# Optimization experiments

Hardware: AMD Instinct MI355X
Metric: run time of the kernel (lower is better)

Reference implementation:

```python
import jax, jax.numpy as jnp
import numpy as np

N, E, D_IN, D_OUT, MAX_DEG = 50000, 800000, 128, 128, 64
ALPHA = 0.5


def _linear_params(key, fan_in, fan_out):
    s = 1.0 / np.sqrt(fan_in)
    kw, kb = jax.random.split(key)
    W = jax.random.uniform(kw, (fan_out, fan_in), jnp.float32, -s, s)
    b = jax.random.uniform(kb, (fan_out,), jnp.float32, -s, s)
    return W, b


def setup_inputs() -> dict:
    key = jax.random.key(0)
    ks = jax.random.split(key, 16)
    x = jax.random.normal(ks[0], (N, D_IN), jnp.float32)
    edge_index = jax.random.randint(ks[1], (2, E), 0, N, dtype=jnp.int64)
    in_degree = jax.random.randint(ks[2], (N,), 0, MAX_DEG, dtype=jnp.int64)
    out_degree = jax.random.randint(ks[3], (N,), 0, MAX_DEG, dtype=jnp.int64)
    out_deg_mask = jax.random.uniform(ks[4], (N,), jnp.float32)
    out_deg_mask_bias = jax.random.uniform(ks[5], (N,), jnp.float32)
    in_deg_mask = jax.random.uniform(ks[6], (N,), jnp.float32)
    in_deg_mask_bias = jax.random.uniform(ks[7], (N,), jnp.float32)
    W_src, b_src = _linear_params(ks[8], D_IN, D_OUT)
    W_dst, b_dst = _linear_params(ks[9], D_IN, D_OUT)
    W_out_f, b_out_f = _linear_params(ks[10], D_IN, 1)
    W_in_f, b_in_f = _linear_params(ks[11], D_IN, 1)
    W_fc, b_fc = _linear_params(ks[12], D_IN, D_OUT)
    # degree embedding tables, padding_idx=0 -> row 0 zeroed
    in_deg_table = (jax.random.normal(ks[13], (MAX_DEG, D_IN), jnp.float32)).at[0].set(0.0)
    out_deg_table = (jax.random.normal(ks[14], (MAX_DEG, D_IN), jnp.float32)).at[0].set(0.0)
    return {
        "x": x, "edge_index": edge_index,
        "in_degree": in_degree, "out_degree": out_degree,
        "out_deg_mask": out_deg_mask, "out_deg_mask_bias": out_deg_mask_bias,
        "in_deg_mask": in_deg_mask, "in_deg_mask_bias": in_deg_mask_bias,
        "W_src": W_src, "b_src": b_src, "W_dst": W_dst, "b_dst": b_dst,
        "W_out_f": W_out_f, "b_out_f": b_out_f, "W_in_f": W_in_f, "b_in_f": b_in_f,
        "W_fc": W_fc, "b_fc": b_fc,
        "in_deg_table": in_deg_table, "out_deg_table": out_deg_table,
    }


def reference(x, edge_index, in_degree, out_degree,
              out_deg_mask, out_deg_mask_bias, in_deg_mask, in_deg_mask_bias,
              W_src, b_src, W_dst, b_dst,
              W_out_f, b_out_f, W_in_f, b_in_f,
              W_fc, b_fc, in_deg_table, out_deg_table):
    n = x.shape[0]
    row, col = edge_index[0], edge_index[1]
    ones = jnp.ones(row.shape[0], x.dtype)
    # directed norm D_out^{-1/2} A D_in^{-1/2}; transpose reuses the same edge weights
    out_deg = jax.ops.segment_sum(ones, row, num_segments=n)
    in_deg = jax.ops.segment_sum(ones, col, num_segments=n)
    o_inv = jnp.where(out_deg > 0, jax.lax.rsqrt(jnp.maximum(out_deg, 1e-12)), 0.0)
    i_inv = jnp.where(in_deg > 0, jax.lax.rsqrt(jnp.maximum(in_deg, 1e-12)), 0.0)
    w = o_inv[row] * i_inv[col]  # [E]
    # adj_norm @ x and adj_t_norm @ x (SpMM via gather + segment_sum)
    out_nei = jax.ops.segment_sum(w[:, None] * x[col], row, num_segments=n)  # [N,D]
    in_nei = jax.ops.segment_sum(w[:, None] * x[row], col, num_segments=n)   # [N,D]
    # degree-gated filter
    c_out = (out_nei - x + out_deg_table[out_degree]) @ W_out_f.T + b_out_f  # [N,1]
    c_in = (in_nei - x + in_deg_table[in_degree]) @ W_in_f.T + b_in_f        # [N,1]
    C = jax.nn.softmax(jnp.concatenate([c_out, c_in], axis=1), axis=1)        # tau_softmax, tau=1
    C_out = C[:, 0:1] * out_deg_mask[:, None] + out_deg_mask_bias[:, None]
    C_in = C[:, 1:2] * in_deg_mask[:, None] + in_deg_mask_bias[:, None]
    out = (C_out * (out_nei @ W_src.T + b_src)
           + C_in * (in_nei @ W_dst.T + b_dst)
           + ALPHA * (x @ W_fc.T + b_fc))
    return out, C_in, C_out
```

## Files before the change

kernel.cpp:

```cpp
#include <hip/hip_runtime.h>

#define NN 50000
#define EE 800000
#define DD 128
#define CAP 48
#define MT 64
#define XSL 6250
#define PB 128
#define PCB (8 * PB)

typedef short short8_t __attribute__((ext_vector_type(8)));
typedef float f32x4 __attribute__((ext_vector_type(4)));
typedef float f32x2 __attribute__((ext_vector_type(2)));

__device__ __forceinline__ unsigned short f2bf(float f) {
    union { float f; unsigned int i; } v; v.f = f;
    unsigned int x = v.i;
    x += 0x7FFFu + ((x >> 16) & 1u);
    return (unsigned short)(x >> 16);
}
__device__ __forceinline__ unsigned int pack2(float a, float b) {
    return (unsigned int)f2bf(a) | ((unsigned int)f2bf(b) << 16);
}
__device__ __forceinline__ f32x2 bfup(unsigned int u) {
    union { unsigned int i; float f; } lo, hi;
    lo.i = u << 16;
    hi.i = u & 0xFFFF0000u;
    f32x2 r; r.x = lo.f; r.y = hi.f;
    return r;
}
__device__ __forceinline__ void pkfma(f32x2& a, f32x2 b, f32x2 w) {
    asm("v_pk_fma_f32 %0, %1, %2, %0" : "+v"(a) : "v"(b), "v"(w));
}
__device__ __forceinline__ void accw(f32x2* ac, uint4 u, float w) {
    f32x2 wp; wp.x = w; wp.y = w;
    pkfma(ac[0], bfup(u.x), wp); pkfma(ac[1], bfup(u.y), wp);
    pkfma(ac[2], bfup(u.z), wp); pkfma(ac[3], bfup(u.w), wp);
}

__global__ void __launch_bounds__(256) k_pc(
    const int* __restrict__ ei, int* __restrict__ cnt,
    unsigned short* __restrict__ bkt_row, unsigned short* __restrict__ bkt_col,
    const float* __restrict__ x,
    const float* __restrict__ W_src, const float* __restrict__ W_dst,
    const float* __restrict__ W_fc,
    unsigned short* __restrict__ xb, unsigned short* __restrict__ wbf)
{
    if (blockIdx.x < PCB) {
        int xcd = blockIdx.x & 7;
        int b   = blockIdx.x >> 3;
        int lo = xcd * XSL, hi = lo + XSL;
        for (int e = b * 256 + threadIdx.x; e < EE; e += PB * 256) {
            int r = __builtin_nontemporal_load(ei + e);
            int c = __builtin_nontemporal_load(ei + EE + e);
            if (r >= lo && r < hi) {
                int po = atomicAdd(&cnt[r], 1);
                if (po < CAP) bkt_row[(size_t)r * CAP + po] = (unsigned short)c;
            }
            if (c >= lo && c < hi) {
                int pi = atomicAdd(&cnt[NN + c], 1);
                if (pi < CAP) bkt_col[(size_t)c * CAP + pi] = (unsigned short)r;
            }
        }
    } else {
        int t = (blockIdx.x - PCB) * 256 + threadIdx.x;
        int base = t * 4;
        if (base < NN * DD) {
            float4 v = *(const float4*)(x + base);
            uint2 p; p.x = pack2(v.x, v.y); p.y = pack2(v.z, v.w);
            *(uint2*)(xb + base) = p;
        } else {
            int b2 = base - NN * DD;
            if (b2 < 3 * 16384) {
                int src = b2 >> 14;
                int off = b2 & 16383;
                const float* W = (src == 0) ? W_src : (src == 1) ? W_dst : W_fc;
                float sc = (src == 2) ? 0.5f : 1.0f;
                float4 v = *(const float4*)(W + off);
                uint2 p; p.x = pack2(v.x * sc, v.y * sc); p.y = pack2(v.z * sc, v.w * sc);
                *(uint2*)(wbf + b2) = p;
            }
        }
    }
}

__global__ void __launch_bounds__(256) k_gather(
    const uint4* __restrict__ xb4, const float4* __restrict__ x4,
    const unsigned short* __restrict__ bkt_row, const unsigned short* __restrict__ bkt_col,
    const int* __restrict__ cnt,
    const int* __restrict__ in_degree, const int* __restrict__ out_degree,
    const float* __restrict__ odm, const float* __restrict__ odmb,
    const float* __restrict__ idm, const float* __restrict__ idmb,
    const float4* __restrict__ W_out_f4, const float* __restrict__ b_out_f,
    const float4* __restrict__ W_in_f4, const float* __restrict__ b_in_f,
    const float4* __restrict__ in_tab4, const float4* __restrict__ out_tab4,
    uint2* __restrict__ onb2, uint2* __restrict__ inb2,
    float* __restrict__ scbuf,
    float* __restrict__ outCin, float* __restrict__ outCout)
{
    __shared__ float4 sred[2][4][2][16][3];
    __shared__ float sg[2][2];
    __shared__ float sC[2][2];
    int half = threadIdx.x >> 7;
    int n = blockIdx.x * 2 + half;
    int t = threadIdx.x & 127;
    int g = t >> 5;
    int l = t & 31;
    int dir = g >> 1;
    int gd  = g & 1;
    int sub = l >> 4;
    int li  = l & 15;
    int shamt = gd << 4;

    const unsigned short* bp = ((dir == 0) ? bkt_row : bkt_col) + (size_t)n * CAP;
    const int* wcnt = (dir == 0) ? (cnt + NN) : cnt;
    int rawdeg = cnt[dir * NN + n];
    int deg = (rawdeg > CAP) ? CAP : rawdeg;

    unsigned int bw = (l < 24) ? *(const unsigned int*)(bp + 2 * l) : 0u;

    float w_l = 0.0f;
    {
        unsigned int pr = __shfl(bw, l >> 1, 32);
        int il = (pr >> ((l & 1) << 4)) & 0xffff;
        if (l < deg) w_l = 1.0f / sqrtf((float)wcnt[il]);
    }

    f32x2 ac[4];
    ac[0] = (f32x2)0.0f; ac[1] = (f32x2)0.0f; ac[2] = (f32x2)0.0f; ac[3] = (f32x2)0.0f;

    if (deg <= 32) {
        int j = gd;
        for (; j + 14 < deg; j += 16) {
            int s0 = j + 2 * sub, s1 = s0 + 4, s2 = s0 + 8, s3 = s0 + 12;
            int i0 = (__shfl(bw, s0 >> 1, 32) >> shamt) & 0xffff;
            int i1 = (__shfl(bw, s1 >> 1, 32) >> shamt) & 0xffff;
            int i2 = (__shfl(bw, s2 >> 1, 32) >> shamt) & 0xffff;
            int i3 = (__shfl(bw, s3 >> 1, 32) >> shamt) & 0xffff;
            uint4 u0 = xb4[(size_t)i0 * 16 + li];
            uint4 u1 = xb4[(size_t)i1 * 16 + li];
            uint4 u2 = xb4[(size_t)i2 * 16 + li];
            uint4 u3 = xb4[(size_t)i3 * 16 + li];
            float w0 = __shfl(w_l, s0, 32);
            float w1 = __shfl(w_l, s1, 32);
            float w2v = __shfl(w_l, s2, 32);
            float w3 = __shfl(w_l, s3, 32);
            accw(ac, u0, w0); accw(ac, u1, w1); accw(ac, u2, w2v); accw(ac, u3, w3);
        }
        for (; j + 6 < deg; j += 8) {
            int s0 = j + 2 * sub, s1 = s0 + 4;
            int i0 = (__shfl(bw, s0 >> 1, 32) >> shamt) & 0xffff;
            int i1 = (__shfl(bw, s1 >> 1, 32) >> shamt) & 0xffff;
            uint4 u0 = xb4[(size_t)i0 * 16 + li];
            uint4 u1 = xb4[(size_t)i1 * 16 + li];
            float w0 = __shfl(w_l, s0, 32);
            float w1 = __shfl(w_l, s1, 32);
            accw(ac, u0, w0); accw(ac, u1, w1);
        }
        for (; j < deg; j += 4) {
            int s0 = j + 2 * sub;
            int sc = (s0 < deg) ? s0 : gd;
            int i0 = (__shfl(bw, sc >> 1, 32) >> shamt) & 0xffff;
            float w0 = __shfl(w_l, sc, 32);
            if (s0 < deg) {
                uint4 u0 = xb4[(size_t)i0 * 16 + li];
                accw(ac, u0, w0);
            }
        }
    } else {
        for (int j = gd; j < deg; j += 4) {
            int s0 = j + 2 * sub;
            int sc = (s0 < deg) ? s0 : gd;
            int i0 = (__shfl(bw, sc >> 1, 32) >> shamt) & 0xffff;
            if (s0 < deg) {
                float w0 = 1.0f / sqrtf((float)wcnt[i0]);
                uint4 u0 = xb4[(size_t)i0 * 16 + li];
                accw(ac, u0, w0);
            }
        }
    }

    sred[half][g][sub][li][0] = make_float4(ac[0].x, ac[0].y, ac[1].x, ac[1].y);
    sred[half][g][sub][li][1] = make_float4(ac[2].x, ac[2].y, ac[3].x, ac[3].y);
    __syncthreads();

    float4 r = make_float4(0.f, 0.f, 0.f, 0.f);
    if (gd == 0) {
        int src = l >> 1, q = l & 1;
        int g0 = dir * 2;
        float4 b0 = sred[half][g0][0][src][q];
        float4 b1 = sred[half][g0][1][src][q];
        float4 b2 = sred[half][g0 + 1][0][src][q];
        float4 b3 = sred[half][g0 + 1][1][src][q];
        float wn = (rawdeg > 0) ? (1.0f / sqrtf((float)rawdeg)) : 0.0f;
        r.x = wn * (b0.x + b1.x + b2.x + b3.x);
        r.y = wn * (b0.y + b1.y + b2.y + b3.y);
        r.z = wn * (b0.z + b1.z + b2.z + b3.z);
        r.w = wn * (b0.w + b1.w + b2.w + b3.w);
        float4 xv = x4[(size_t)n * 32 + l];
        float4 tb, wf;
        if (dir == 0) {
            int odg = out_degree[n];
            odg = (odg < 0) ? 0 : (odg > 63 ? 63 : odg);
            tb = out_tab4[(size_t)odg * 32 + l];
            wf = W_out_f4[l];
        } else {
            int idg = in_degree[n];
            idg = (idg < 0) ? 0 : (idg > 63 ? 63 : idg);
            tb = in_tab4[(size_t)idg * 32 + l];
            wf = W_in_f4[l];
        }
        float p = (r.x - xv.x + tb.x) * wf.x + (r.y - xv.y + tb.y) * wf.y
                + (r.z - xv.z + tb.z) * wf.z + (r.w - xv.w + tb.w) * wf.w;
        #pragma unroll
        for (int off = 16; off > 0; off >>= 1) p += __shfl_down(p, off);
        if (l == 0) sg[half][dir] = p;
    }
    __syncthreads();
    if (t == 0) {
        float c_out = sg[half][0] + b_out_f[0];
        float c_in  = sg[half][1] + b_in_f[0];
        float m  = fmaxf(c_out, c_in);
        float eo = expf(c_out - m);
        float e2 = expf(c_in  - m);
        float inv = 1.0f / (eo + e2);
        float Cout = (eo * inv) * odm[n] + odmb[n];
        float Cin  = (e2 * inv) * idm[n] + idmb[n];
        sC[half][0] = Cout; sC[half][1] = Cin;
        scbuf[2 * n]     = Cout;
        scbuf[2 * n + 1] = Cin;
        outCout[n] = Cout;
        outCin[n]  = Cin;
    }
    __syncthreads();
    if (gd == 0) {
        float C = sC[half][dir];
        uint2 pw; pw.x = pack2(C * r.x, C * r.y); pw.y = pack2(C * r.z, C * r.w);
        ((dir == 0) ? onb2 : inb2)[(size_t)n * 32 + l] = pw;
    }
}

__global__ void __launch_bounds__(256) k_gemm(
    const unsigned int* __restrict__ xb32,
    const unsigned int* __restrict__ onb32, const unsigned int* __restrict__ inb32,
    const unsigned short* __restrict__ wbf,
    const float* __restrict__ b_src, const float* __restrict__ b_dst,
    const float* __restrict__ b_fc,
    const float* __restrict__ scbuf,
    float* __restrict__ out)
{
    __shared__ unsigned short sA[MT * 72];
    __shared__ unsigned short sBt[DD * 72];

    int tid = threadIdx.x;
    int wid = tid >> 6;
    int lane = tid & 63;
    int ml = lane & 15;
    int kq = lane >> 4;
    int n0 = blockIdx.x * MT;

    f32x4 accv[8];
    #pragma unroll
    for (int i = 0; i < 8; i++) accv[i] = (f32x4)0.0f;

    const unsigned int* srcs[3] = { onb32, inb32, xb32 };

    for (int kt = 0; kt < 6; kt++) {
        int srcsel = kt >> 1;
        int k0 = (kt & 1) * 64;
        const unsigned int* S = srcs[srcsel];

        #pragma unroll
        for (int r = 0; r < 2; r++) {
            int s = tid + 256 * r;
            int row = s >> 3;
            int cg = s & 7;
            int gn = n0 + row;
            uint4 p = make_uint4(0u, 0u, 0u, 0u);
            if (gn < NN) {
                p = *(const uint4*)(S + (size_t)gn * 64 + (k0 >> 1) + cg * 4);
            }
            *(uint4*)(sA + row * 72 + cg * 8) = p;
        }
        #pragma unroll
        for (int r = 0; r < 4; r++) {
            int s = tid + 256 * r;
            int row = s >> 3;
            int cg = s & 7;
            uint4 w = *(const uint4*)(wbf + srcsel * 16384 + row * DD + k0 + cg * 8);
            *(uint4*)(sBt + row * 72 + cg * 8) = w;
        }
        __syncthreads();

        #pragma unroll
        for (int ks = 0; ks < 64; ks += 32) {
            short8_t a = *(const short8_t*)(sA + (16 * wid + ml) * 72 + ks + kq * 8);
            #pragma unroll
            for (int i = 0; i < 8; i++) {
                short8_t b = *(const short8_t*)(sBt + (16 * i + ml) * 72 + ks + kq * 8);
                accv[i] = __builtin_amdgcn_mfma_f32_16x16x32_bf16(a, b, accv[i], 0, 0, 0);
            }
        }
        __syncthreads();
    }

    int row_base = n0 + 16 * wid + 4 * kq;
    #pragma unroll
    for (int r = 0; r < 4; r++) {
        int row = row_base + r;
        if (row >= NN) continue;
        float Cout = scbuf[2 * row];
        float Cin  = scbuf[2 * row + 1];
        #pragma unroll
        for (int i = 0; i < 8; i++) {
            int col = 16 * i + ml;
            out[(size_t)row * DD + col] =
                accv[i][r] + Cout * b_src[col] + Cin * b_dst[col] + 0.5f * b_fc[col];
        }
    }
}

extern "C" void kernel_launch(void* const* d_in, const int* in_sizes, int n_in,
                              void* d_out, int out_size, void* d_ws, size_t ws_size,
                              hipStream_t stream) {
    const float* x    = (const float*)d_in[0];
    const int* ei     = (const int*)d_in[1];
    const int* in_degree  = (const int*)d_in[2];
    const int* out_degree = (const int*)d_in[3];
    const float* odm  = (const float*)d_in[4];
    const float* odmb = (const float*)d_in[5];
    const float* idm  = (const float*)d_in[6];
    const float* idmb = (const float*)d_in[7];
    const float* W_src = (const float*)d_in[8];
    const float* b_src = (const float*)d_in[9];
    const float* W_dst = (const float*)d_in[10];
    const float* b_dst = (const float*)d_in[11];
    const float* W_out_f = (const float*)d_in[12];
    const float* b_out_f = (const float*)d_in[13];
    const float* W_in_f  = (const float*)d_in[14];
    const float* b_in_f  = (const float*)d_in[15];
    const float* W_fc    = (const float*)d_in[16];
    const float* b_fc    = (const float*)d_in[17];
    const float* in_tab  = (const float*)d_in[18];
    const float* out_tab = (const float*)d_in[19];

    unsigned short* xb  = (unsigned short*)d_ws;
    unsigned short* onb = xb + (size_t)NN * DD;
    unsigned short* inb = onb + (size_t)NN * DD;
    float* scbuf = (float*)(inb + (size_t)NN * DD);
    unsigned short* wbf = (unsigned short*)(scbuf + 2 * NN);
    int* cnt     = (int*)(wbf + 3 * 16384);
    unsigned short* bkt_row = (unsigned short*)(cnt + 2 * NN);
    unsigned short* bkt_col = bkt_row + (size_t)NN * CAP;

    hipMemsetAsync(cnt, 0, (size_t)2 * NN * sizeof(int), stream);

    int conv_quads = (NN * DD + 3 * 16384) / 4;
    int conv_blocks = (conv_quads + 255) / 256;
    k_pc<<<PCB + conv_blocks, 256, 0, stream>>>(ei, cnt, bkt_row, bkt_col,
                                                x, W_src, W_dst, W_fc, xb, wbf);

    float* out_p  = (float*)d_out;
    float* cin_p  = out_p + (size_t)NN * DD;
    float* cout_p = cin_p + NN;

    k_gather<<<NN / 2, 256, 0, stream>>>((const uint4*)xb, (const float4*)x,
                                         bkt_row, bkt_col, cnt,
                                         in_degree, out_degree,
                                         odm, odmb, idm, idmb,
                                         (const float4*)W_out_f, b_out_f,
                                         (const float4*)W_in_f, b_in_f,
                                         (const float4*)in_tab, (const float4*)out_tab,
                                         (uint2*)onb, (uint2*)inb,
                                         scbuf, cin_p, cout_p);

    k_gemm<<<(NN + MT - 1) / MT, 256, 0, stream>>>(
        (const unsigned int*)xb, (const unsigned int*)onb, (const unsigned int*)inb,
        wbf, b_src, b_dst, b_fc, scbuf, out_p);
}
```

Before: 282.5 us.

## Merge memset, placement/conversion and gather into one cooperative persistent kernel

Replaces the memset, the edge-bucketing/conversion kernel and the per-node gather kernel with a single cooperative kernel. It zeroes the counters, places edges and converts to bf16, then runs a grid-stride gather loop, with grid.sync between phases. This removes launch gaps and the memset. In exchange the grid is capped at 2048 blocks, fewer than before for the placement and conversion phases, the placement loads lose their nontemporal hints, and grid-wide barriers are added. A fallback to separate kernels is kept in case the cooperative launch fails.

```diff
diff --git a/kernel.cpp b/kernel.cpp
--- a/kernel.cpp
+++ b/kernel.cpp
@@ -1,4 +1,6 @@
 #include <hip/hip_runtime.h>
+#include <hip/hip_cooperative_groups.h>
+namespace cg = cooperative_groups;
 
 #define NN 50000
 #define EE 800000
@@ -6,8 +8,6 @@
 #define CAP 48
 #define MT 64
 #define XSL 6250
-#define PB 128
-#define PCB (8 * PB)
 
 typedef short short8_t __attribute__((ext_vector_type(8)));
 typedef float f32x4 __attribute__((ext_vector_type(4)));
@@ -38,53 +38,62 @@
     pkfma(ac[2], bfup(u.z), wp); pkfma(ac[3], bfup(u.w), wp);
 }
 
-__global__ void __launch_bounds__(256) k_pc(
-    const int* __restrict__ ei, int* __restrict__ cnt,
-    unsigned short* __restrict__ bkt_row, unsigned short* __restrict__ bkt_col,
-    const float* __restrict__ x,
+struct GShared {
+    float4 sred[2][4][2][16][3];
+    float sg[2][2];
+    float sC[2][2];
+};
+
+
+__device__ __forceinline__ void place_phase(
+    int bid, int P, int tid, const int* __restrict__ ei, int* __restrict__ cnt,
+    unsigned short* __restrict__ bkt_row, unsigned short* __restrict__ bkt_col)
+{
+    int xcd = bid & 7;
+    int b   = bid >> 3;
+    int PBd = P >> 3;
+    int lo = xcd * XSL, hi = lo + XSL;
+    for (int e = b * 256 + tid; e < EE; e += PBd * 256) {
+        int r = ei[e];
+        int c = ei[EE + e];
+        if (r >= lo && r < hi) {
+            int po = atomicAdd(&cnt[r], 1);
+            if (po < CAP) bkt_row[(size_t)r * CAP + po] = (unsigned short)c;
+        }
+        if (c >= lo && c < hi) {
+            int pi = atomicAdd(&cnt[NN + c], 1);
+            if (pi < CAP) bkt_col[(size_t)c * CAP + pi] = (unsigned short)r;
+        }
+    }
+}
+
+#define QT ((NN * DD + 3 * 16384) / 4)
+
+__device__ __forceinline__ void conv_work(
+    int q, const float* __restrict__ x,
     const float* __restrict__ W_src, const float* __restrict__ W_dst,
     const float* __restrict__ W_fc,
     unsigned short* __restrict__ xb, unsigned short* __restrict__ wbf)
 {
-    if (blockIdx.x < PCB) {
-        int xcd = blockIdx.x & 7;
-        int b   = blockIdx.x >> 3;
-        int lo = xcd * XSL, hi = lo + XSL;
-        for (int e = b * 256 + threadIdx.x; e < EE; e += PB * 256) {
-            int r = __builtin_nontemporal_load(ei + e);
-            int c = __builtin_nontemporal_load(ei + EE + e);
-            if (r >= lo && r < hi) {
-                int po = atomicAdd(&cnt[r], 1);
-                if (po < CAP) bkt_row[(size_t)r * CAP + po] = (unsigned short)c;
-            }
-            if (c >= lo && c < hi) {
-                int pi = atomicAdd(&cnt[NN + c], 1);
-                if (pi < CAP) bkt_col[(size_t)c * CAP + pi] = (unsigned short)r;
-            }
-        }
+    int base = q * 4;
+    if (base < NN * DD) {
+        float4 v = *(const float4*)(x + base);
+        uint2 p; p.x = pack2(v.x, v.y); p.y = pack2(v.z, v.w);
+        *(uint2*)(xb + base) = p;
     } else {
-        int t = (blockIdx.x - PCB) * 256 + threadIdx.x;
-        int base = t * 4;
-        if (base < NN * DD) {
-            float4 v = *(const float4*)(x + base);
-            uint2 p; p.x = pack2(v.x, v.y); p.y = pack2(v.z, v.w);
-            *(uint2*)(xb + base) = p;
-        } else {
-            int b2 = base - NN * DD;
-            if (b2 < 3 * 16384) {
-                int src = b2 >> 14;
-                int off = b2 & 16383;
-                const float* W = (src == 0) ? W_src : (src == 1) ? W_dst : W_fc;
-                float sc = (src == 2) ? 0.5f : 1.0f;
-                float4 v = *(const float4*)(W + off);
-                uint2 p; p.x = pack2(v.x * sc, v.y * sc); p.y = pack2(v.z * sc, v.w * sc);
-                *(uint2*)(wbf + b2) = p;
-            }
-        }
-    }
-}
-
-__global__ void __launch_bounds__(256) k_gather(
+        int b2 = base - NN * DD;
+        int src = b2 >> 14;
+        int off = b2 & 16383;
+        const float* W = (src == 0) ? W_src : (src == 1) ? W_dst : W_fc;
+        float sc = (src == 2) ? 0.5f : 1.0f;
+        float4 v = *(const float4*)(W + off);
+        uint2 p; p.x = pack2(v.x * sc, v.y * sc); p.y = pack2(v.z * sc, v.w * sc);
+        *(uint2*)(wbf + b2) = p;
+    }
+}
+
+__device__ __forceinline__ void gather_pair(
+    GShared& sh, int p,
     const uint4* __restrict__ xb4, const float4* __restrict__ x4,
     const unsigned short* __restrict__ bkt_row, const unsigned short* __restrict__ bkt_col,
     const int* __restrict__ cnt,
@@ -98,11 +107,8 @@
     float* __restrict__ scbuf,
     float* __restrict__ outCin, float* __restrict__ outCout)
 {
-    __shared__ float4 sred[2][4][2][16][3];
-    __shared__ float sg[2][2];
-    __shared__ float sC[2][2];
     int half = threadIdx.x >> 7;
-    int n = blockIdx.x * 2 + half;
+    int n = p * 2 + half;
     int t = threadIdx.x & 127;
     int g = t >> 5;
     int l = t & 31;
@@ -180,18 +186,18 @@
         }
     }
 
-    sred[half][g][sub][li][0] = make_float4(ac[0].x, ac[0].y, ac[1].x, ac[1].y);
-    sred[half][g][sub][li][1] = make_float4(ac[2].x, ac[2].y, ac[3].x, ac[3].y);
+    sh.sred[half][g][sub][li][0] = make_float4(ac[0].x, ac[0].y, ac[1].x, ac[1].y);
+    sh.sred[half][g][sub][li][1] = make_float4(ac[2].x, ac[2].y, ac[3].x, ac[3].y);
     __syncthreads();
 
     float4 r = make_float4(0.f, 0.f, 0.f, 0.f);
     if (gd == 0) {
         int src = l >> 1, q = l & 1;
         int g0 = dir * 2;
-        float4 b0 = sred[half][g0][0][src][q];
-        float4 b1 = sred[half][g0][1][src][q];
-        float4 b2 = sred[half][g0 + 1][0][src][q];
-        float4 b3 = sred[half][g0 + 1][1][src][q];
+        float4 b0 = sh.sred[half][g0][0][src][q];
+        float4 b1 = sh.sred[half][g0][1][src][q];
+        float4 b2 = sh.sred[half][g0 + 1][0][src][q];
+        float4 b3 = sh.sred[half][g0 + 1][1][src][q];
         float wn = (rawdeg > 0) ? (1.0f / sqrtf((float)rawdeg)) : 0.0f;
         r.x = wn * (b0.x + b1.x + b2.x + b3.x);
         r.y = wn * (b0.y + b1.y + b2.y + b3.y);
@@ -210,23 +216,23 @@
             tb = in_tab4[(size_t)idg * 32 + l];
             wf = W_in_f4[l];
         }
-        float p = (r.x - xv.x + tb.x) * wf.x + (r.y - xv.y + tb.y) * wf.y
-                + (r.z - xv.z + tb.z) * wf.z + (r.w - xv.w + tb.w) * wf.w;
+        float pv = (r.x - xv.x + tb.x) * wf.x + (r.y - xv.y + tb.y) * wf.y
+                 + (r.z - xv.z + tb.z) * wf.z + (r.w - xv.w + tb.w) * wf.w;
         #pragma unroll
-        for (int off = 16; off > 0; off >>= 1) p += __shfl_down(p, off);
-        if (l == 0) sg[half][dir] = p;
+        for (int off = 16; off > 0; off >>= 1) pv += __shfl_down(pv, off);
+        if (l == 0) sh.sg[half][dir] = pv;
     }
     __syncthreads();
     if (t == 0) {
-        float c_out = sg[half][0] + b_out_f[0];
-        float c_in  = sg[half][1] + b_in_f[0];
+        float c_out = sh.sg[half][0] + b_out_f[0];
+        float c_in  = sh.sg[half][1] + b_in_f[0];
         float m  = fmaxf(c_out, c_in);
         float eo = expf(c_out - m);
         float e2 = expf(c_in  - m);
         float inv = 1.0f / (eo + e2);
         float Cout = (eo * inv) * odm[n] + odmb[n];
         float Cin  = (e2 * inv) * idm[n] + idmb[n];
-        sC[half][0] = Cout; sC[half][1] = Cin;
+        sh.sC[half][0] = Cout; sh.sC[half][1] = Cin;
         scbuf[2 * n]     = Cout;
         scbuf[2 * n + 1] = Cin;
         outCout[n] = Cout;
@@ -234,10 +240,93 @@
     }
     __syncthreads();
     if (gd == 0) {
-        float C = sC[half][dir];
+        float C = sh.sC[half][dir];
         uint2 pw; pw.x = pack2(C * r.x, C * r.y); pw.y = pack2(C * r.z, C * r.w);
         ((dir == 0) ? onb2 : inb2)[(size_t)n * 32 + l] = pw;
     }
+}
+
+__global__ void __launch_bounds__(256) k_main(
+    const int* __restrict__ ei, int* __restrict__ cnt,
+    unsigned short* __restrict__ bkt_row, unsigned short* __restrict__ bkt_col,
+    const float* __restrict__ x,
+    const float* __restrict__ W_src, const float* __restrict__ W_dst,
+    const float* __restrict__ W_fc,
+    unsigned short* __restrict__ xb, unsigned short* __restrict__ wbf,
+    const int* __restrict__ in_degree, const int* __restrict__ out_degree,
+    const float* __restrict__ odm, const float* __restrict__ odmb,
+    const float* __restrict__ idm, const float* __restrict__ idmb,
+    const float* __restrict__ W_out_f, const float* __restrict__ b_out_f,
+    const float* __restrict__ W_in_f, const float* __restrict__ b_in_f,
+    const float* __restrict__ in_tab, const float* __restrict__ out_tab,
+    uint2* __restrict__ onb2, uint2* __restrict__ inb2,
+    float* __restrict__ scbuf,
+    float* __restrict__ outCin, float* __restrict__ outCout)
+{
+    cg::grid_group grid = cg::this_grid();
+    __shared__ GShared sh;
+    int tid = threadIdx.x;
+    int G = gridDim.x;
+
+    for (int i = blockIdx.x * 256 + tid; i < 2 * NN; i += G * 256) cnt[i] = 0;
+    grid.sync();
+
+    int P = G >> 1;
+    if ((int)blockIdx.x < P) {
+        place_phase(blockIdx.x, P, tid, ei, cnt, bkt_row, bkt_col);
+    } else {
+        int CB = G - P;
+        for (int q = (blockIdx.x - P) * 256 + tid; q < QT; q += CB * 256)
+            conv_work(q, x, W_src, W_dst, W_fc, xb, wbf);
+    }
+    grid.sync();
+
+    for (int p = blockIdx.x; p < NN / 2; p += G)
+        gather_pair(sh, p, (const uint4*)xb, (const float4*)x, bkt_row, bkt_col,
+                    cnt, in_degree, out_degree, odm, odmb, idm, idmb,
+                    (const float4*)W_out_f, b_out_f, (const float4*)W_in_f, b_in_f,
+                    (const float4*)in_tab, (const float4*)out_tab,
+                    onb2, inb2, scbuf, outCin, outCout);
+}
+
+#define FPCB 1024
+__global__ void __launch_bounds__(256) k_pc_f(
+    const int* __restrict__ ei, int* __restrict__ cnt,
+    unsigned short* __restrict__ bkt_row, unsigned short* __restrict__ bkt_col,
+    const float* __restrict__ x,
+    const float* __restrict__ W_src, const float* __restrict__ W_dst,
+    const float* __restrict__ W_fc,
+    unsigned short* __restrict__ xb, unsigned short* __restrict__ wbf)
+{
+    if (blockIdx.x < FPCB) {
+        place_phase(blockIdx.x, FPCB, threadIdx.x, ei, cnt, bkt_row, bkt_col);
+    } else {
+        int q = (blockIdx.x - FPCB) * 256 + threadIdx.x;
+        if (q < QT) conv_work(q, x, W_src, W_dst, W_fc, xb, wbf);
+    }
+}
+
+__global__ void __launch_bounds__(256) k_gather_f(
+    const int* __restrict__ ei_unused,
+    const unsigned short* __restrict__ bkt_row, const unsigned short* __restrict__ bkt_col,
+    const int* __restrict__ cnt, const float* __restrict__ x,
+    const unsigned short* __restrict__ xb,
+    const int* __restrict__ in_degree, const int* __restrict__ out_degree,
+    const float* __restrict__ odm, const float* __restrict__ odmb,
+    const float* __restrict__ idm, const float* __restrict__ idmb,
+    const float* __restrict__ W_out_f, const float* __restrict__ b_out_f,
+    const float* __restrict__ W_in_f, const float* __restrict__ b_in_f,
+    const float* __restrict__ in_tab, const float* __restrict__ out_tab,
+    uint2* __restrict__ onb2, uint2* __restrict__ inb2,
+    float* __restrict__ scbuf,
+    float* __restrict__ outCin, float* __restrict__ outCout)
+{
+    __shared__ GShared sh;
+    gather_pair(sh, blockIdx.x, (const uint4*)xb, (const float4*)x, bkt_row, bkt_col,
+                cnt, in_degree, out_degree, odm, odmb, idm, idmb,
+                (const float4*)W_out_f, b_out_f, (const float4*)W_in_f, b_in_f,
+                (const float4*)in_tab, (const float4*)out_tab,
+                onb2, inb2, scbuf, outCin, outCout);
 }
 
 __global__ void __launch_bounds__(256) k_gemm(
@@ -274,21 +363,21 @@
         for (int r = 0; r < 2; r++) {
             int s = tid + 256 * r;
             int row = s >> 3;
-            int cg = s & 7;
+            int cg2 = s & 7;
             int gn = n0 + row;
             uint4 p = make_uint4(0u, 0u, 0u, 0u);
             if (gn < NN) {
-                p = *(const uint4*)(S + (size_t)gn * 64 + (k0 >> 1) + cg * 4);
+                p = *(const uint4*)(S + (size_t)gn * 64 + (k0 >> 1) + cg2 * 4);
             }
-            *(uint4*)(sA + row * 72 + cg * 8) = p;
+            *(uint4*)(sA + row * 72 + cg2 * 8) = p;
         }
         #pragma unroll
         for (int r = 0; r < 4; r++) {
             int s = tid + 256 * r;
             int row = s >> 3;
-            int cg = s & 7;
-            uint4 w = *(const uint4*)(wbf + srcsel * 16384 + row * DD + k0 + cg * 8);
-            *(uint4*)(sBt + row * 72 + cg * 8) = w;
+            int cg2 = s & 7;
+            uint4 w = *(const uint4*)(wbf + srcsel * 16384 + row * DD + k0 + cg2 * 8);
+            *(uint4*)(sBt + row * 72 + cg2 * 8) = w;
         }
         __syncthreads();
 
@@ -353,26 +442,46 @@
     unsigned short* bkt_row = (unsigned short*)(cnt + 2 * NN);
     unsigned short* bkt_col = bkt_row + (size_t)NN * CAP;
 
-    hipMemsetAsync(cnt, 0, (size_t)2 * NN * sizeof(int), stream);
-
-    int conv_quads = (NN * DD + 3 * 16384) / 4;
-    int conv_blocks = (conv_quads + 255) / 256;
-    k_pc<<<PCB + conv_blocks, 256, 0, stream>>>(ei, cnt, bkt_row, bkt_col,
-                                                x, W_src, W_dst, W_fc, xb, wbf);
-
     float* out_p  = (float*)d_out;
     float* cin_p  = out_p + (size_t)NN * DD;
     float* cout_p = cin_p + NN;
 
-    k_gather<<<NN / 2, 256, 0, stream>>>((const uint4*)xb, (const float4*)x,
-                                         bkt_row, bkt_col, cnt,
-                                         in_degree, out_degree,
-                                         odm, odmb, idm, idmb,
-                                         (const float4*)W_out_f, b_out_f,
-                                         (const float4*)W_in_f, b_in_f,
-                                         (const float4*)in_tab, (const float4*)out_tab,
-                                         (uint2*)onb, (uint2*)inb,
-                                         scbuf, cin_p, cout_p);
+    uint2* onb2 = (uint2*)onb;
+    uint2* inb2 = (uint2*)inb;
+
+    int nb = 0;
+    hipOccupancyMaxActiveBlocksPerMultiprocessor(&nb, k_main, 256, 0);
+    if (nb < 1) nb = 1;
+    long grid_l = (long)nb * 256;
+    if (grid_l > 2048) grid_l = 2048;
+    int grid = ((int)grid_l) & ~15;
+    if (grid < 16) grid = 16;
+
+    void* args[] = {
+        (void*)&ei, (void*)&cnt, (void*)&bkt_row, (void*)&bkt_col,
+        (void*)&x, (void*)&W_src, (void*)&W_dst, (void*)&W_fc,
+        (void*)&xb, (void*)&wbf,
+        (void*)&in_degree, (void*)&out_degree,
+        (void*)&odm, (void*)&odmb, (void*)&idm, (void*)&idmb,
+        (void*)&W_out_f, (void*)&b_out_f, (void*)&W_in_f, (void*)&b_in_f,
+        (void*)&in_tab, (void*)&out_tab,
+        (void*)&onb2, (void*)&inb2, (void*)&scbuf,
+        (void*)&cin_p, (void*)&cout_p
+    };
+    hipError_t err = hipLaunchCooperativeKernel((void*)k_main, dim3(grid), dim3(256),
+                                                args, 0, stream);
+    if (err != hipSuccess) {
+        hipMemsetAsync(cnt, 0, (size_t)2 * NN * sizeof(int), stream);
+        int conv_blocks = (QT + 255) / 256;
+        k_pc_f<<<FPCB + conv_blocks, 256, 0, stream>>>(ei, cnt, bkt_row, bkt_col,
+                                                       x, W_src, W_dst, W_fc, xb, wbf);
+        k_gather_f<<<NN / 2, 256, 0, stream>>>(ei, bkt_row, bkt_col, cnt, x, xb,
+                                               in_degree, out_degree,
+                                               odm, odmb, idm, idmb,
+                                               W_out_f, b_out_f, W_in_f, b_in_f,
+                                               in_tab, out_tab,
+                                               onb2, inb2, scbuf, cin_p, cout_p);
+    }
 
     k_gemm<<<(NN + MT - 1) / MT, 256, 0, stream>>>(
         (const unsigned int*)xb, (const unsigned int*)onb, (const unsigned int*)inb,
```

Result: slower. 565.8 us (+100.3%).
